# Kernel tuning notes

Hardware: AMD Instinct MI355X
Metric: run time of the kernel (lower is better)

## Reference

```python
import jax, jax.numpy as jnp
import numpy as np

B, S, DIM = 2, 2048, 2048
H, KVH, HD = 16, 8, 128
NREP = H // KVH


def _make_freqs(seqlen, head_dim):
    # Rotation-matrix form of RoPE: freqs[s,0,p] = [[cos,-sin],[sin,cos]]
    pos = jnp.arange(seqlen, dtype=jnp.float32)
    inv = 1.0 / (10000.0 ** (jnp.arange(0, head_dim, 2, dtype=jnp.float32) / head_dim))
    ang = pos[:, None] * inv[None, :]                      # (S, HD/2)
    cos, sin = jnp.cos(ang), jnp.sin(ang)
    f = jnp.stack([jnp.stack([cos, -sin], -1),
                   jnp.stack([sin, cos], -1)], -2)          # (S, HD/2, 2, 2)
    return f[:, None]                                       # (S, 1, HD/2, 2, 2)


def setup_inputs() -> dict:
    key = jax.random.key(0)
    k0, k1, k2, k3, k4 = jax.random.split(key, 5)
    x = jax.random.normal(k0, (B, S, DIM), jnp.float32)
    x_mask = jnp.ones((B, S), jnp.bool_)                    # unused by forward
    freqs_cis = _make_freqs(S, HD)
    w_qkv = jax.random.normal(k1, ((H + 2 * KVH) * HD, DIM), jnp.float32) * (DIM ** -0.5)
    w_out = jax.random.normal(k2, (DIM, H * HD), jnp.float32) * ((H * HD) ** -0.5)
    q_norm_w = 1.0 + 0.02 * jax.random.normal(k3, (HD,), jnp.float32)
    k_norm_w = 1.0 + 0.02 * jax.random.normal(k4, (HD,), jnp.float32)
    return {"x": x, "x_mask": x_mask, "freqs_cis": freqs_cis,
            "w_qkv": w_qkv, "w_out": w_out,
            "q_norm_w": q_norm_w, "k_norm_w": k_norm_w}


def _rmsnorm(x, w):
    eps = jnp.asarray(jnp.finfo(x.dtype).eps, x.dtype)
    return x * jax.lax.rsqrt(jnp.mean(x * x, -1, keepdims=True) + eps) * w


def _rope(x, freqs):
    # x: (B,S,h,HD), freqs: (S,1,HD/2,2,2)
    t = x.reshape(*x.shape[:-1], HD // 2, 1, 2)
    out = freqs[..., 0] * t[..., 0] + freqs[..., 1] * t[..., 1]
    return out.reshape(x.shape)


def reference(x, x_mask, freqs_cis, w_qkv, w_out, q_norm_w, k_norm_w):
    b, s, _ = x.shape
    qkv = jnp.einsum('bsd,od->bso', x, w_qkv)
    xq, xk, xv = jnp.split(qkv, [H * HD, (H + KVH) * HD], axis=-1)
    xq = _rope(_rmsnorm(xq.reshape(b, s, H, HD), q_norm_w), freqs_cis)
    xk = _rope(_rmsnorm(xk.reshape(b, s, KVH, HD), k_norm_w), freqs_cis)
    xv = xv.reshape(b, s, KVH, HD)
    # GQA: repeat kv heads (consecutive copies, matching unsqueeze+repeat+flatten)
    xk = jnp.repeat(xk, NREP, axis=2)
    xv = jnp.repeat(xv, NREP, axis=2)
    scale = HD ** -0.5
    scores = jnp.einsum('bqhd,bkhd->bhqk', xq, xk) * scale
    attn = jax.nn.softmax(scores, axis=-1)
    out = jnp.einsum('bhqk,bkhd->bqhd', attn, xv).reshape(b, s, H * HD)
    return jnp.einsum('bso,do->bsd', out, w_out)
```

## Files before the change

kernel.cpp:

```cpp
#include <hip/hip_runtime.h>
#include <hip/hip_bf16.h>
#include <cstdint>

typedef __bf16 bf16_t;
typedef __attribute__((ext_vector_type(8)))  __bf16 bf16x8;
typedef __attribute__((ext_vector_type(4)))  float  f32x4;
typedef __attribute__((ext_vector_type(16))) float  f32x16;

#define AS1 __attribute__((address_space(1)))
#define AS3 __attribute__((address_space(3)))
#define DEV __device__ __forceinline__

#define S_BARRIER() asm volatile("s_barrier" ::: "memory")
#define VMCNT0()    asm volatile("s_waitcnt vmcnt(0)" ::: "memory")
#define VMCNT4()    asm volatile("s_waitcnt vmcnt(4)" ::: "memory")
#define VMCNT8()    asm volatile("s_waitcnt vmcnt(8)" ::: "memory")
#define SCHED0()    __builtin_amdgcn_sched_barrier(0)

#if __has_builtin(__builtin_amdgcn_exp2f)
#define EXP2(x) __builtin_amdgcn_exp2f(x)
#else
#define EXP2(x) exp2f(x)
#endif

DEV uint32_t pk2bf(float lo, float hi) {
  union { __bf16 h[2]; uint32_t u; } x;
  x.h[0] = (__bf16)lo; x.h[1] = (__bf16)hi; return x.u;
}

__global__ __launch_bounds__(256) void k_cvt3(const float* __restrict__ s0,
                                              const float* __restrict__ s1,
                                              const float* __restrict__ s2,
                                              bf16_t* __restrict__ dst) {
  long i = (long)(blockIdx.x * 256 + threadIdx.x) * 4;
  const float* src;
  long off;
  if (i < 8388608)        { src = s0; off = i; }
  else if (i < 16777216)  { src = s1; off = i - 8388608; }
  else                    { src = s2; off = i - 16777216; }
  const float4 v = *reinterpret_cast<const float4*>(src + off);
  union { bf16_t h[4]; uint2 u; } o;
  o.h[0] = (bf16_t)v.x; o.h[1] = (bf16_t)v.y;
  o.h[2] = (bf16_t)v.z; o.h[3] = (bf16_t)v.w;
  *reinterpret_cast<uint2*>(dst + i) = o.u;
}

#define RD_A4(dst, base, MF)                                              \
  _Pragma("unroll") for (int j_ = 0; j_ < 4; ++j_)                        \
  _Pragma("unroll") for (int kk_ = 0; kk_ < 2; ++kk_) {                   \
    int p_ = (wm*128 + ((MF)+j_)*16 + c16)*128 + kk_*64 + g*16;           \
    p_ ^= ((p_>>9)&1)<<5;                                                 \
    dst[j_][kk_] = *reinterpret_cast<const bf16x8*>((const char*)(base) + p_); }

#define RD_B_ALL(dst, base)                                               \
  _Pragma("unroll") for (int i_ = 0; i_ < 4; ++i_)                        \
  _Pragma("unroll") for (int kk_ = 0; kk_ < 2; ++kk_) {                   \
    int p_ = (wn*64 + i_*16 + c16)*128 + kk_*64 + g*16;                   \
    p_ ^= ((p_>>9)&1)<<5;                                                 \
    dst[i_][kk_] = *reinterpret_cast<const bf16x8*>((const char*)(base) + p_); }

#define RD_B2(dst, base)                                                  \
  _Pragma("unroll") for (int i_ = 0; i_ < 2; ++i_)                        \
  _Pragma("unroll") for (int kk_ = 0; kk_ < 2; ++kk_) {                   \
    int p_ = (wn*32 + i_*16 + c16)*128 + kk_*64 + g*16;                   \
    p_ ^= ((p_>>9)&1)<<5;                                                 \
    dst[i_][kk_] = *reinterpret_cast<const bf16x8*>((const char*)(base) + p_); }

#define MM_Q(aa, MB, NB)                                                  \
  _Pragma("unroll") for (int j_ = 0; j_ < 4; ++j_)                        \
  _Pragma("unroll") for (int i_ = 0; i_ < 2; ++i_)                        \
  _Pragma("unroll") for (int kk_ = 0; kk_ < 2; ++kk_)                     \
    acc[(MB)+j_][(NB)+i_] = __builtin_amdgcn_mfma_f32_16x16x32_bf16(      \
        aa[j_][kk_], bF[(NB)+i_][kk_], acc[(MB)+j_][(NB)+i_], 0, 0, 0);

#define MM_OG(aa, MB)                                                     \
  _Pragma("unroll") for (int j_ = 0; j_ < 4; ++j_)                        \
  _Pragma("unroll") for (int i_ = 0; i_ < 2; ++i_)                        \
  _Pragma("unroll") for (int kk_ = 0; kk_ < 2; ++kk_)                     \
    acc[(MB)+j_][i_] = __builtin_amdgcn_mfma_f32_16x16x32_bf16(           \
        aa[j_][kk_], bG[i_][kk_], acc[(MB)+j_][i_], 0, 0, 0);

#define STAGE_A(dstbase, half, tt)                                        \
  _Pragma("unroll") for (int j_ = 0; j_ < 2; ++j_)                        \
    __builtin_amdgcn_global_load_lds(                                     \
        (const AS1 void*)(Ag + srcA[half][j_] + (tt)*64),                 \
        (AS3 void*)((char*)(dstbase) + ((half)*1024 + 512*j_ + wuni)*16), \
        16, 0, 0);

#define STAGE_B(dstbase, half, tt)                                        \
  _Pragma("unroll") for (int j_ = 0; j_ < 2; ++j_)                        \
    __builtin_amdgcn_global_load_lds(                                     \
        (const AS1 void*)(Bg + srcB[half][j_] + (tt)*64),                 \
        (AS3 void*)((char*)(dstbase) + ((half)*1024 + 512*j_ + wuni)*16), \
        16, 0, 0);

#define STAGE_B2(dstbase, tt)                                             \
  _Pragma("unroll") for (int j_ = 0; j_ < 2; ++j_)                        \
    __builtin_amdgcn_global_load_lds(                                     \
        (const AS1 void*)(Bg + srcB2[j_] + (tt)*64),                      \
        (AS3 void*)((char*)(dstbase) + (512*j_ + wuni)*16), 16, 0, 0);

__global__ __launch_bounds__(512, 2) void k_gemm256(
    const bf16_t* __restrict__ Ag, const bf16_t* __restrict__ Bg,
    void* __restrict__ Cv, int M, int N, int K, int out_bf16)
{
  extern __shared__ char smemraw[];
  const int tid = threadIdx.x;
  const int w = tid >> 6, l = tid & 63;
  const int wm = w >> 2, wn = w & 3;
  const int c16 = l & 15, g = l >> 4;
  const int wuni = tid & 0x1C0;

  const int nwg = gridDim.x, cpx = nwg >> 3;
  const int bid = blockIdx.x;
  const int L = (bid & 7) * cpx + (bid >> 3);
  const int nbx = N >> 8;
  const int m0 = (L / nbx) * 256, n0 = (L % nbx) * 256;

  int srcA[2][2], srcB[2][2];
#pragma unroll
  for (int half = 0; half < 2; ++half)
#pragma unroll
    for (int j = 0; j < 2; ++j) {
      int ch = half * 1024 + 512 * j + tid;
      int cc = ch ^ (((ch >> 5) & 1) << 1);
      int row = cc >> 3, c8 = (cc & 7) * 8;
      srcA[half][j] = (m0 + row) * K + c8;
      srcB[half][j] = (n0 + row) * K + c8;
    }

  f32x4 acc[8][4] = {};
  bf16x8 aF[4][2], bF[4][2];

  char* const Ab0 = smemraw;
  char* const Ab1 = smemraw + 32768;
  char* const Bb0 = smemraw + 65536;
  char* const Bb1 = smemraw + 98304;

  const int NT = K >> 6;

  STAGE_B(Bb0, 0, 0); STAGE_B(Bb0, 1, 0);
  STAGE_A(Ab0, 0, 0); STAGE_A(Ab0, 1, 0);
  VMCNT0();
  S_BARRIER();
  RD_B_ALL(bF, Bb0);

#pragma unroll 1
  for (int t = 0; t < NT; ++t) {
    char* const Asp = (t & 1) ? Ab1 : Ab0;
    char* const Asn = (t & 1) ? Ab0 : Ab1;
    char* const Bsn = (t & 1) ? Bb0 : Bb1;
    const bool more = (t + 1 < NT);

    VMCNT0();
    if (more) { STAGE_B(Bsn, 0, t + 1); }
    S_BARRIER();
    RD_A4(aF, Asp, 0);
    __builtin_amdgcn_s_setprio(1);
    MM_Q(aF, 0, 0);
    __builtin_amdgcn_s_setprio(0); SCHED0();
    S_BARRIER();

    if (more) { STAGE_B(Bsn, 1, t + 1); }
    S_BARRIER();
    __builtin_amdgcn_s_setprio(1);
    MM_Q(aF, 0, 2);
    __builtin_amdgcn_s_setprio(0); SCHED0();
    S_BARRIER();

    if (more) { STAGE_A(Asn, 0, t + 1); }
    S_BARRIER();
    RD_A4(aF, Asp, 4);
    __builtin_amdgcn_s_setprio(1);
    MM_Q(aF, 4, 0);
    __builtin_amdgcn_s_setprio(0); SCHED0();
    S_BARRIER();

    if (more) { STAGE_A(Asn, 1, t + 1); VMCNT4(); }
    S_BARRIER();
    __builtin_amdgcn_s_setprio(1);
    MM_Q(aF, 4, 2);
    __builtin_amdgcn_s_setprio(0); SCHED0();
    if (more) { RD_B_ALL(bF, Bsn); }
    S_BARRIER();
  }

#pragma unroll
  for (int mf = 0; mf < 8; ++mf)
#pragma unroll
    for (int nf = 0; nf < 4; ++nf) {
      const int cc = n0 + wn * 64 + nf * 16 + c16;
#pragma unroll
      for (int r = 0; r < 4; ++r) {
        const int rr = m0 + wm * 128 + mf * 16 + g * 4 + r;
        if (out_bf16)
          ((bf16_t*)Cv)[(size_t)rr * N + cc] = (bf16_t)acc[mf][nf][r];
        else
          ((float*)Cv)[(size_t)rr * N + cc] = acc[mf][nf][r];
      }
    }
}

__global__ __launch_bounds__(512, 2) void k_og(
    const bf16_t* __restrict__ Ag, const bf16_t* __restrict__ Bg,
    float* __restrict__ Cv, int M, int N, int K)
{
  extern __shared__ char smemraw[];
  const int tid = threadIdx.x;
  const int w = tid >> 6, l = tid & 63;
  const int wm = w >> 2, wn = w & 3;
  const int c16 = l & 15, g = l >> 4;
  const int wuni = tid & 0x1C0;

  const int nwg = gridDim.x, cpx = nwg >> 3;
  const int bid = blockIdx.x;
  const int L = (bid & 7) * cpx + (bid >> 3);
  const int nbx = N >> 7;
  const int m0 = (L / nbx) * 256, n0 = (L % nbx) * 128;

  int srcA[2][2], srcB2[2];
#pragma unroll
  for (int half = 0; half < 2; ++half)
#pragma unroll
    for (int j = 0; j < 2; ++j) {
      int ch = half * 1024 + 512 * j + tid;
      int cc = ch ^ (((ch >> 5) & 1) << 1);
      int row = cc >> 3, c8 = (cc & 7) * 8;
      srcA[half][j] = (m0 + row) * K + c8;
    }
#pragma unroll
  for (int j = 0; j < 2; ++j) {
    int ch = 512 * j + tid;
    int cc = ch ^ (((ch >> 5) & 1) << 1);
    int row = cc >> 3, c8 = (cc & 7) * 8;
    srcB2[j] = (n0 + row) * K + c8;
  }

  f32x4 acc[8][2] = {};
  bf16x8 aF[4][2], bG[2][2];

  char* const Ab0 = smemraw;
  char* const Ab1 = smemraw + 32768;
  char* const Bb0 = smemraw + 65536;
  char* const Bb1 = smemraw + 81920;

  const int NT = K >> 6;

  STAGE_B2(Bb0, 0);
  STAGE_A(Ab0, 0, 0); STAGE_A(Ab0, 1, 0);
  VMCNT0();
  S_BARRIER();
  RD_B2(bG, Bb0);

#pragma unroll 1
  for (int t = 0; t < NT; ++t) {
    char* const Asp = (t & 1) ? Ab1 : Ab0;
    char* const Asn = (t & 1) ? Ab0 : Ab1;
    char* const Bsn = (t & 1) ? Bb0 : Bb1;
    const bool more = (t + 1 < NT);

    VMCNT0();
    if (more) { STAGE_B2(Bsn, t + 1); STAGE_A(Asn, 0, t + 1); }
    S_BARRIER();
    RD_A4(aF, Asp, 0);
    __builtin_amdgcn_s_setprio(1);
    MM_OG(aF, 0);
    __builtin_amdgcn_s_setprio(0); SCHED0();
    S_BARRIER();

    if (more) { STAGE_A(Asn, 1, t + 1); VMCNT4(); }
    S_BARRIER();
    RD_A4(aF, Asp, 4);
    __builtin_amdgcn_s_setprio(1);
    MM_OG(aF, 4);
    __builtin_amdgcn_s_setprio(0); SCHED0();
    if (more) { RD_B2(bG, Bsn); }
    S_BARRIER();
  }

#pragma unroll
  for (int mf = 0; mf < 8; ++mf)
#pragma unroll
    for (int nf = 0; nf < 2; ++nf) {
      const int cc = n0 + wn * 32 + nf * 16 + c16;
#pragma unroll
      for (int r = 0; r < 4; ++r) {
        const int rr = m0 + wm * 128 + mf * 16 + g * 4 + r;
        Cv[(size_t)rr * N + cc] = acc[mf][nf][r];
      }
    }
}

__global__ __launch_bounds__(256) void k_prep(
    const bf16_t* __restrict__ qkv, const float* __restrict__ freqs,
    const float* __restrict__ qw, const float* __restrict__ kw,
    bf16_t* __restrict__ Qd, bf16_t* __restrict__ Kd,
    bf16_t* __restrict__ Vt)
{
  __shared__ bf16_t vt[64][136];
  const int bid = blockIdx.x;
  if (bid < 24576) {
    const int w = threadIdx.x >> 6, l = threadIdx.x & 63;
    const int R = bid * 4 + w;
    const int j = R >> 12;
    const int token = R & 4095;
    const int s = token & 2047, b = token >> 11;
    const bool isq = (j < 16);
    const int col0 = isq ? (j << 7) : (2048 + ((j - 16) << 7));

    union { uint32_t u; __bf16 h[2]; } xin;
    xin.u = *reinterpret_cast<const uint32_t*>(qkv + (size_t)token * 4096 + col0 + 2 * l);
    float x0 = (float)xin.h[0], x1 = (float)xin.h[1];
    float ss = x0 * x0 + x1 * x1;
#pragma unroll
    for (int d = 1; d < 64; d <<= 1) ss += __shfl_xor(ss, d, 64);
    const float rn = rsqrtf(ss * (1.0f / 128.0f) + 1.1920929e-7f);
    const float2 wv = *reinterpret_cast<const float2*>((isq ? qw : kw) + 2 * l);
    const float y0 = x0 * rn * wv.x, y1 = x1 * rn * wv.y;
    const float4 f = *reinterpret_cast<const float4*>(freqs + (size_t)s * 256 + l * 4);
    float o0 = f.x * y0 + f.y * y1;
    float o1 = f.z * y0 + f.w * y1;
    if (isq) { o0 *= 0.1275187989014331f; o1 *= 0.1275187989014331f; }
    const uint32_t pk = pk2bf(o0, o1);
    if (isq)
      *reinterpret_cast<uint32_t*>(Qd + ((size_t)(b * 16 + j) * 2048 + s) * 128 + 2 * l) = pk;
    else
      *reinterpret_cast<uint32_t*>(Kd + ((size_t)(b * 8 + (j - 16)) * 2048 + s) * 128 + 2 * l) = pk;
  } else {
    const int vb = bid - 24576;
    const int tid = threadIdx.x;
    const int st = vb & 31, kh = (vb >> 5) & 7, b = vb >> 8;
    const int s0 = st * 64;
#pragma unroll
    for (int i = 0; i < 4; ++i) {
      int ch = tid + 256 * i;
      int srow = ch >> 4, d8 = ch & 15;
      bf16x8 v = *reinterpret_cast<const bf16x8*>(
          qkv + (size_t)(b * 2048 + s0 + srow) * 4096 + 3072 + kh * 128 + d8 * 8);
      *reinterpret_cast<bf16x8*>(&vt[srow][d8 * 8]) = v;
    }
    __syncthreads();
    const int d = tid >> 1, sc = tid & 1;
    bf16_t* dst = Vt + ((size_t)(b * 8 + kh) * 128 + d) * 2048 + s0 + 32 * sc;
#pragma unroll
    for (int grp = 0; grp < 4; ++grp) {
      uint32_t pk[4];
#pragma unroll
      for (int q = 0; q < 4; ++q) {
        int jj = 32 * sc + grp * 8 + q * 2;
        union { __bf16 h[2]; uint32_t u; } e;
        e.h[0] = vt[jj][d]; e.h[1] = vt[jj + 1][d];
        pk[q] = e.u;
      }
      uint4 o; o.x = pk[0]; o.y = pk[1]; o.z = pk[2]; o.w = pk[3];
      *reinterpret_cast<uint4*>(dst + grp * 8) = o;
    }
  }
}

__global__ __launch_bounds__(256, 2) void k_attn(
    const bf16_t* __restrict__ Qd, const bf16_t* __restrict__ Kd,
    const bf16_t* __restrict__ Vt, bf16_t* __restrict__ O)
{
  __shared__ bf16_t kbuf[2][64 * 128];
  __shared__ bf16_t vbuf[2][128 * 64];
  const int tid = threadIdx.x;
  const int w = tid >> 6, l = tid & 63;
  const int c = l & 31, h2 = l >> 5;
  const int bid = blockIdx.x;
  const int qt = bid & 15, h = (bid >> 4) & 15, b = bid >> 8;
  const int kvh = h >> 1;
  const bf16_t* Qg = Qd + ((size_t)(b * 16 + h) * 2048 + qt * 128 + w * 32) * 128;
  const bf16_t* Kg = Kd + ((size_t)(b * 8 + kvh) * 2048) * 128;
  const bf16_t* Vg = Vt + ((size_t)(b * 8 + kvh) * 128) * 2048;

  bf16x8 qf[8];
#pragma unroll
  for (int s = 0; s < 8; ++s)
    qf[s] = *reinterpret_cast<const bf16x8*>(Qg + (size_t)c * 128 + s * 16 + h2 * 8);

  f32x16 oacc[4] = {};
  float l0 = 0.f, l1 = 0.f, l2 = 0.f, l3 = 0.f;

  auto stage = [&](int buf, int kt) {
#pragma unroll
    for (int i = 0; i < 4; ++i) {
      int ch = tid + 256 * i;
      {
        int key = ch >> 4, d16 = ch & 15;
        int soff = key * 256 + ((d16 * 16) ^ ((key & 7) << 4));
        __builtin_amdgcn_global_load_lds(
            (const AS1 void*)((const char*)Kg + (size_t)kt * 64 * 256 + soff),
            (AS3 void*)((char*)&kbuf[buf][0] + (w * 64 + 256 * i) * 16), 16, 0, 0);
      }
      {
        int d = ch >> 3, k8 = (ch & 7) ^ (d & 7);
        __builtin_amdgcn_global_load_lds(
            (const AS1 void*)(Vg + (size_t)d * 2048 + kt * 64 + k8 * 8),
            (AS3 void*)((char*)&vbuf[buf][0] + (w * 64 + 256 * i) * 16), 16, 0, 0);
      }
    }
  };

  auto compute = [&](int buf) {
    f32x16 sacc[2] = {};
    const char* kb = (const char*)&kbuf[buf][0];
    __builtin_amdgcn_s_setprio(1);
#pragma unroll
    for (int m = 0; m < 2; ++m)
#pragma unroll
      for (int s = 0; s < 8; ++s) {
        int byte = (m * 32 + c) * 256 + ((s * 32 + h2 * 16) ^ ((c & 7) << 4));
        bf16x8 kf = *reinterpret_cast<const bf16x8*>(kb + byte);
        sacc[m] = __builtin_amdgcn_mfma_f32_32x32x16_bf16(kf, qf[s], sacc[m], 0, 0, 0);
      }
    __builtin_amdgcn_s_setprio(0);

#pragma unroll
    for (int m = 0; m < 2; ++m)
#pragma unroll
      for (int r = 0; r < 16; r += 4) {
        float p0 = EXP2(sacc[m][r + 0]);
        float p1 = EXP2(sacc[m][r + 1]);
        float p2 = EXP2(sacc[m][r + 2]);
        float p3 = EXP2(sacc[m][r + 3]);
        sacc[m][r + 0] = p0; sacc[m][r + 1] = p1;
        sacc[m][r + 2] = p2; sacc[m][r + 3] = p3;
        l0 += p0; l1 += p1; l2 += p2; l3 += p3;
      }

    const char* vb = (const char*)&vbuf[buf][0];
#pragma unroll
    for (int t = 0; t < 4; ++t) {
      const int m = t >> 1, q2i = t & 1;
      uint32_t u0 = pk2bf(sacc[m][8 * q2i + 0], sacc[m][8 * q2i + 1]);
      uint32_t u1 = pk2bf(sacc[m][8 * q2i + 2], sacc[m][8 * q2i + 3]);
      uint32_t u2 = pk2bf(sacc[m][8 * q2i + 4], sacc[m][8 * q2i + 5]);
      uint32_t u3 = pk2bf(sacc[m][8 * q2i + 6], sacc[m][8 * q2i + 7]);
      auto r02 = __builtin_amdgcn_permlane32_swap((int)u0, (int)u2, false, false);
      auto r13 = __builtin_amdgcn_permlane32_swap((int)u1, (int)u3, false, false);
      union { uint32_t u[4]; bf16x8 v; } pb;
      pb.u[0] = (uint32_t)r02[0]; pb.u[1] = (uint32_t)r13[0];
      pb.u[2] = (uint32_t)r02[1]; pb.u[3] = (uint32_t)r13[1];
      __builtin_amdgcn_s_setprio(1);
#pragma unroll
      for (int df = 0; df < 4; ++df) {
        int byte = (df * 32 + c) * 128 + ((t * 32 + h2 * 16) ^ ((c & 7) << 4));
        bf16x8 vf = *reinterpret_cast<const bf16x8*>(vb + byte);
        oacc[df] = __builtin_amdgcn_mfma_f32_32x32x16_bf16(vf, pb.v, oacc[df], 0, 0, 0);
      }
      __builtin_amdgcn_s_setprio(0);
    }
  };

  stage(0, 0);
#pragma unroll 1
  for (int kt = 0; kt < 31; ++kt) {
    stage((kt + 1) & 1, kt + 1);
    VMCNT8();
    S_BARRIER();
    compute(kt & 1);
    S_BARRIER();
  }
  VMCNT0();
  S_BARRIER();
  compute(1);

  float lrun = (l0 + l1) + (l2 + l3);
  lrun += __shfl_xor(lrun, 32, 64);
  const float inv = 1.0f / lrun;
  bf16_t* Og = O + ((size_t)(b * 2048 + qt * 128 + w * 32 + c) * 2048) + h * 128;
#pragma unroll
  for (int df = 0; df < 4; ++df)
#pragma unroll
    for (int rg = 0; rg < 4; ++rg) {
      uint32_t w0 = pk2bf(oacc[df][rg * 4 + 0] * inv, oacc[df][rg * 4 + 1] * inv);
      uint32_t w1 = pk2bf(oacc[df][rg * 4 + 2] * inv, oacc[df][rg * 4 + 3] * inv);
      uint2 ww; ww.x = w0; ww.y = w1;
      *reinterpret_cast<uint2*>(Og + df * 32 + 8 * rg + 4 * h2) = ww;
    }
}

extern "C" void kernel_launch(void* const* d_in, const int* in_sizes, int n_in,
                              void* d_out, int out_size, void* d_ws, size_t ws_size,
                              hipStream_t stream)
{
  const float* x     = (const float*)d_in[0];
  const float* freqs = (const float*)d_in[2];
  const float* wqkv  = (const float*)d_in[3];
  const float* wout  = (const float*)d_in[4];
  const float* qw    = (const float*)d_in[5];
  const float* kw    = (const float*)d_in[6];
  float* out = (float*)d_out;

  bf16_t* Xb   = (bf16_t*)d_ws;
  bf16_t* Wqb  = Xb  + 8388608;
  bf16_t* Wob  = Wqb + 8388608;
  bf16_t* qkvb = Wob + 4194304;
  bf16_t* Qdp  = qkvb + 16777216;
  bf16_t* Kdp  = Qdp + 8388608;
  bf16_t* Vtp  = Kdp + 4194304;
  bf16_t* Ob   = qkvb;

  (void)hipFuncSetAttribute((const void*)k_gemm256,
                            hipFuncAttributeMaxDynamicSharedMemorySize, 131072);
  (void)hipFuncSetAttribute((const void*)k_og,
                            hipFuncAttributeMaxDynamicSharedMemorySize, 98304);

  k_cvt3<<<20480, 256, 0, stream>>>(x, wqkv, wout, Xb);
  k_gemm256<<<256, 512, 131072, stream>>>(Xb, Wqb, qkvb, 4096, 4096, 2048, 1);
  k_prep<<<25088, 256, 0, stream>>>(qkvb, freqs, qw, kw, Qdp, Kdp, Vtp);
  k_attn<<<512, 256, 0, stream>>>(Qdp, Kdp, Vtp, Ob);
  k_og<<<256, 512, 98304, stream>>>(Ob, Wob, out, 4096, 2048, 2048);
}
```

Baseline: 232.8 us.

## Process two 32-row query tiles per warp in attention, halving warps per block

The attention kernel now runs 2 warps per block instead of 4, and each warp handles 64 query rows as two 32-row MFMA tiles. Each K/V fragment read from LDS therefore feeds two MFMAs, halving LDS read traffic per unit of compute. Each thread issues twice as many async global-to-LDS loads, so the vmcnt wait is raised to match. The cost is doubled register use (two sets of Q fragments, score and output accumulators) and fewer waves per CU to hide latency, with launch bounds changed to (128,1).

Result: slower. 249.8 us (+7.3%).

```diff
diff --git a/kernel.cpp b/kernel.cpp
--- a/kernel.cpp
+++ b/kernel.cpp
@@ -14,7 +14,7 @@
 #define S_BARRIER() asm volatile("s_barrier" ::: "memory")
 #define VMCNT0()    asm volatile("s_waitcnt vmcnt(0)" ::: "memory")
 #define VMCNT4()    asm volatile("s_waitcnt vmcnt(4)" ::: "memory")
-#define VMCNT8()    asm volatile("s_waitcnt vmcnt(8)" ::: "memory")
+#define VMCNT16()   asm volatile("s_waitcnt vmcnt(16)" ::: "memory")
 #define SCHED0()    __builtin_amdgcn_sched_barrier(0)
 
 #if __has_builtin(__builtin_amdgcn_exp2f)
@@ -358,7 +358,7 @@
   }
 }
 
-__global__ __launch_bounds__(256, 2) void k_attn(
+__global__ __launch_bounds__(128, 1) void k_attn(
     const bf16_t* __restrict__ Qd, const bf16_t* __restrict__ Kd,
     const bf16_t* __restrict__ Vt, bf16_t* __restrict__ O)
 {
@@ -370,40 +370,43 @@
   const int bid = blockIdx.x;
   const int qt = bid & 15, h = (bid >> 4) & 15, b = bid >> 8;
   const int kvh = h >> 1;
-  const bf16_t* Qg = Qd + ((size_t)(b * 16 + h) * 2048 + qt * 128 + w * 32) * 128;
+  const bf16_t* Qg = Qd + ((size_t)(b * 16 + h) * 2048 + qt * 128 + w * 64) * 128;
   const bf16_t* Kg = Kd + ((size_t)(b * 8 + kvh) * 2048) * 128;
   const bf16_t* Vg = Vt + ((size_t)(b * 8 + kvh) * 128) * 2048;
 
-  bf16x8 qf[8];
-#pragma unroll
-  for (int s = 0; s < 8; ++s)
-    qf[s] = *reinterpret_cast<const bf16x8*>(Qg + (size_t)c * 128 + s * 16 + h2 * 8);
-
-  f32x16 oacc[4] = {};
-  float l0 = 0.f, l1 = 0.f, l2 = 0.f, l3 = 0.f;
+  bf16x8 qf0[8], qf1[8];
+#pragma unroll
+  for (int s = 0; s < 8; ++s) {
+    qf0[s] = *reinterpret_cast<const bf16x8*>(Qg + (size_t)c * 128 + s * 16 + h2 * 8);
+    qf1[s] = *reinterpret_cast<const bf16x8*>(Qg + (size_t)(32 + c) * 128 + s * 16 + h2 * 8);
+  }
+
+  f32x16 oacc0[4] = {}, oacc1[4] = {};
+  float la0 = 0.f, la1 = 0.f, la2 = 0.f, la3 = 0.f;
+  float lb0 = 0.f, lb1 = 0.f, lb2 = 0.f, lb3 = 0.f;
 
   auto stage = [&](int buf, int kt) {
 #pragma unroll
-    for (int i = 0; i < 4; ++i) {
-      int ch = tid + 256 * i;
+    for (int i = 0; i < 8; ++i) {
+      int ch = tid + 128 * i;
       {
         int key = ch >> 4, d16 = ch & 15;
         int soff = key * 256 + ((d16 * 16) ^ ((key & 7) << 4));
         __builtin_amdgcn_global_load_lds(
             (const AS1 void*)((const char*)Kg + (size_t)kt * 64 * 256 + soff),
-            (AS3 void*)((char*)&kbuf[buf][0] + (w * 64 + 256 * i) * 16), 16, 0, 0);
+            (AS3 void*)((char*)&kbuf[buf][0] + ch * 16), 16, 0, 0);
       }
       {
         int d = ch >> 3, k8 = (ch & 7) ^ (d & 7);
         __builtin_amdgcn_global_load_lds(
             (const AS1 void*)(Vg + (size_t)d * 2048 + kt * 64 + k8 * 8),
-            (AS3 void*)((char*)&vbuf[buf][0] + (w * 64 + 256 * i) * 16), 16, 0, 0);
+            (AS3 void*)((char*)&vbuf[buf][0] + ch * 16), 16, 0, 0);
       }
     }
   };
 
   auto compute = [&](int buf) {
-    f32x16 sacc[2] = {};
+    f32x16 s0[2] = {}, s1[2] = {};
     const char* kb = (const char*)&kbuf[buf][0];
     __builtin_amdgcn_s_setprio(1);
 #pragma unroll
@@ -412,7 +415,8 @@
       for (int s = 0; s < 8; ++s) {
         int byte = (m * 32 + c) * 256 + ((s * 32 + h2 * 16) ^ ((c & 7) << 4));
         bf16x8 kf = *reinterpret_cast<const bf16x8*>(kb + byte);
-        sacc[m] = __builtin_amdgcn_mfma_f32_32x32x16_bf16(kf, qf[s], sacc[m], 0, 0, 0);
+        s0[m] = __builtin_amdgcn_mfma_f32_32x32x16_bf16(kf, qf0[s], s0[m], 0, 0, 0);
+        s1[m] = __builtin_amdgcn_mfma_f32_32x32x16_bf16(kf, qf1[s], s1[m], 0, 0, 0);
       }
     __builtin_amdgcn_s_setprio(0);
 
@@ -420,34 +424,49 @@
     for (int m = 0; m < 2; ++m)
 #pragma unroll
       for (int r = 0; r < 16; r += 4) {
-        float p0 = EXP2(sacc[m][r + 0]);
-        float p1 = EXP2(sacc[m][r + 1]);
-        float p2 = EXP2(sacc[m][r + 2]);
-        float p3 = EXP2(sacc[m][r + 3]);
-        sacc[m][r + 0] = p0; sacc[m][r + 1] = p1;
-        sacc[m][r + 2] = p2; sacc[m][r + 3] = p3;
-        l0 += p0; l1 += p1; l2 += p2; l3 += p3;
+        float a0 = EXP2(s0[m][r + 0]);
+        float a1 = EXP2(s0[m][r + 1]);
+        float a2 = EXP2(s0[m][r + 2]);
+        float a3 = EXP2(s0[m][r + 3]);
+        s0[m][r + 0] = a0; s0[m][r + 1] = a1; s0[m][r + 2] = a2; s0[m][r + 3] = a3;
+        la0 += a0; la1 += a1; la2 += a2; la3 += a3;
+        float b0 = EXP2(s1[m][r + 0]);
+        float b1 = EXP2(s1[m][r + 1]);
+        float b2 = EXP2(s1[m][r + 2]);
+        float b3 = EXP2(s1[m][r + 3]);
+        s1[m][r + 0] = b0; s1[m][r + 1] = b1; s1[m][r + 2] = b2; s1[m][r + 3] = b3;
+        lb0 += b0; lb1 += b1; lb2 += b2; lb3 += b3;
       }
 
     const char* vb = (const char*)&vbuf[buf][0];
 #pragma unroll
     for (int t = 0; t < 4; ++t) {
       const int m = t >> 1, q2i = t & 1;
-      uint32_t u0 = pk2bf(sacc[m][8 * q2i + 0], sacc[m][8 * q2i + 1]);
-      uint32_t u1 = pk2bf(sacc[m][8 * q2i + 2], sacc[m][8 * q2i + 3]);
-      uint32_t u2 = pk2bf(sacc[m][8 * q2i + 4], sacc[m][8 * q2i + 5]);
-      uint32_t u3 = pk2bf(sacc[m][8 * q2i + 6], sacc[m][8 * q2i + 7]);
+      uint32_t u0 = pk2bf(s0[m][8 * q2i + 0], s0[m][8 * q2i + 1]);
+      uint32_t u1 = pk2bf(s0[m][8 * q2i + 2], s0[m][8 * q2i + 3]);
+      uint32_t u2 = pk2bf(s0[m][8 * q2i + 4], s0[m][8 * q2i + 5]);
+      uint32_t u3 = pk2bf(s0[m][8 * q2i + 6], s0[m][8 * q2i + 7]);
       auto r02 = __builtin_amdgcn_permlane32_swap((int)u0, (int)u2, false, false);
       auto r13 = __builtin_amdgcn_permlane32_swap((int)u1, (int)u3, false, false);
-      union { uint32_t u[4]; bf16x8 v; } pb;
-      pb.u[0] = (uint32_t)r02[0]; pb.u[1] = (uint32_t)r13[0];
-      pb.u[2] = (uint32_t)r02[1]; pb.u[3] = (uint32_t)r13[1];
+      union { uint32_t u[4]; bf16x8 v; } pb0;
+      pb0.u[0] = (uint32_t)r02[0]; pb0.u[1] = (uint32_t)r13[0];
+      pb0.u[2] = (uint32_t)r02[1]; pb0.u[3] = (uint32_t)r13[1];
+      uint32_t w0 = pk2bf(s1[m][8 * q2i + 0], s1[m][8 * q2i + 1]);
+      uint32_t w1 = pk2bf(s1[m][8 * q2i + 2], s1[m][8 * q2i + 3]);
+      uint32_t w2 = pk2bf(s1[m][8 * q2i + 4], s1[m][8 * q2i + 5]);
+      uint32_t w3 = pk2bf(s1[m][8 * q2i + 6], s1[m][8 * q2i + 7]);
+      auto t02 = __builtin_amdgcn_permlane32_swap((int)w0, (int)w2, false, false);
+      auto t13 = __builtin_amdgcn_permlane32_swap((int)w1, (int)w3, false, false);
+      union { uint32_t u[4]; bf16x8 v; } pb1;
+      pb1.u[0] = (uint32_t)t02[0]; pb1.u[1] = (uint32_t)t13[0];
+      pb1.u[2] = (uint32_t)t02[1]; pb1.u[3] = (uint32_t)t13[1];
       __builtin_amdgcn_s_setprio(1);
 #pragma unroll
       for (int df = 0; df < 4; ++df) {
         int byte = (df * 32 + c) * 128 + ((t * 32 + h2 * 16) ^ ((c & 7) << 4));
         bf16x8 vf = *reinterpret_cast<const bf16x8*>(vb + byte);
-        oacc[df] = __builtin_amdgcn_mfma_f32_32x32x16_bf16(vf, pb.v, oacc[df], 0, 0, 0);
+        oacc0[df] = __builtin_amdgcn_mfma_f32_32x32x16_bf16(vf, pb0.v, oacc0[df], 0, 0, 0);
+        oacc1[df] = __builtin_amdgcn_mfma_f32_32x32x16_bf16(vf, pb1.v, oacc1[df], 0, 0, 0);
       }
       __builtin_amdgcn_s_setprio(0);
     }
@@ -457,7 +476,7 @@
 #pragma unroll 1
   for (int kt = 0; kt < 31; ++kt) {
     stage((kt + 1) & 1, kt + 1);
-    VMCNT8();
+    VMCNT16();
     S_BARRIER();
     compute(kt & 1);
     S_BARRIER();
@@ -466,18 +485,26 @@
   S_BARRIER();
   compute(1);
 
-  float lrun = (l0 + l1) + (l2 + l3);
-  lrun += __shfl_xor(lrun, 32, 64);
-  const float inv = 1.0f / lrun;
-  bf16_t* Og = O + ((size_t)(b * 2048 + qt * 128 + w * 32 + c) * 2048) + h * 128;
+  float lrun0 = (la0 + la1) + (la2 + la3);
+  lrun0 += __shfl_xor(lrun0, 32, 64);
+  float lrun1 = (lb0 + lb1) + (lb2 + lb3);
+  lrun1 += __shfl_xor(lrun1, 32, 64);
+  const float inv0 = 1.0f / lrun0;
+  const float inv1 = 1.0f / lrun1;
+  bf16_t* Og0 = O + ((size_t)(b * 2048 + qt * 128 + w * 64 + c) * 2048) + h * 128;
+  bf16_t* Og1 = Og0 + (size_t)32 * 2048;
 #pragma unroll
   for (int df = 0; df < 4; ++df)
 #pragma unroll
     for (int rg = 0; rg < 4; ++rg) {
-      uint32_t w0 = pk2bf(oacc[df][rg * 4 + 0] * inv, oacc[df][rg * 4 + 1] * inv);
-      uint32_t w1 = pk2bf(oacc[df][rg * 4 + 2] * inv, oacc[df][rg * 4 + 3] * inv);
-      uint2 ww; ww.x = w0; ww.y = w1;
-      *reinterpret_cast<uint2*>(Og + df * 32 + 8 * rg + 4 * h2) = ww;
+      uint32_t a0 = pk2bf(oacc0[df][rg * 4 + 0] * inv0, oacc0[df][rg * 4 + 1] * inv0);
+      uint32_t a1 = pk2bf(oacc0[df][rg * 4 + 2] * inv0, oacc0[df][rg * 4 + 3] * inv0);
+      uint2 wa; wa.x = a0; wa.y = a1;
+      *reinterpret_cast<uint2*>(Og0 + df * 32 + 8 * rg + 4 * h2) = wa;
+      uint32_t b0w = pk2bf(oacc1[df][rg * 4 + 0] * inv1, oacc1[df][rg * 4 + 1] * inv1);
+      uint32_t b1w = pk2bf(oacc1[df][rg * 4 + 2] * inv1, oacc1[df][rg * 4 + 3] * inv1);
+      uint2 wb; wb.x = b0w; wb.y = b1w;
+      *reinterpret_cast<uint2*>(Og1 + df * 32 + 8 * rg + 4 * h2) = wb;
     }
 }
 
@@ -510,6 +537,6 @@
   k_cvt3<<<20480, 256, 0, stream>>>(x, wqkv, wout, Xb);
   k_gemm256<<<256, 512, 131072, stream>>>(Xb, Wqb, qkvb, 4096, 4096, 2048, 1);
   k_prep<<<25088, 256, 0, stream>>>(qkvb, freqs, qw, kw, Qdp, Kdp, Vtp);
-  k_attn<<<512, 256, 0, stream>>>(Qdp, Kdp, Vtp, Ob);
+  k_attn<<<512, 128, 0, stream>>>(Qdp, Kdp, Vtp, Ob);
   k_og<<<256, 512, 98304, stream>>>(Ob, Wob, out, 4096, 2048, 2048);
 }
```

## Triple-buffer A tiles in QKV GEMM to prefetch two K-steps ahead

Applied to the files above, without the earlier changes.

The QKV projection GEMM moves from double-buffered A and B LDS tiles to a three-slot ring for A, with A loads issued two iterations ahead while B stays one ahead. The blanket vmcnt(0) wait at the top of each iteration is dropped in favour of partial waits, so global loads can stay in flight across more compute. This needs 160KB of dynamic LDS instead of 128KB and makes the wait-count bookkeeping more delicate. If the counts are wrong, tiles could be read before they arrive.

After: 234.1 us. No clear change (+0.6%).

```diff
diff --git a/kernel.cpp b/kernel.cpp
--- a/kernel.cpp
+++ b/kernel.cpp
@@ -132,28 +132,29 @@
   f32x4 acc[8][4] = {};
   bf16x8 aF[4][2], bF[4][2];
 
-  char* const Ab0 = smemraw;
-  char* const Ab1 = smemraw + 32768;
-  char* const Bb0 = smemraw + 65536;
-  char* const Bb1 = smemraw + 98304;
+  char* const Ab = smemraw;
+  char* const Bb = smemraw + 98304;
 
   const int NT = K >> 6;
 
-  STAGE_B(Bb0, 0, 0); STAGE_B(Bb0, 1, 0);
-  STAGE_A(Ab0, 0, 0); STAGE_A(Ab0, 1, 0);
-  VMCNT0();
+  STAGE_B(Bb, 0, 0); STAGE_B(Bb, 1, 0);
+  STAGE_A(Ab, 0, 0); STAGE_A(Ab, 1, 0);
+  STAGE_A(Ab + 32768, 0, 1); STAGE_A(Ab + 32768, 1, 1);
+  VMCNT4();
   S_BARRIER();
-  RD_B_ALL(bF, Bb0);
-
+  RD_B_ALL(bF, Bb);
+
+  int aCur = 0;
 #pragma unroll 1
   for (int t = 0; t < NT; ++t) {
-    char* const Asp = (t & 1) ? Ab1 : Ab0;
-    char* const Asn = (t & 1) ? Ab0 : Ab1;
-    char* const Bsn = (t & 1) ? Bb0 : Bb1;
-    const bool more = (t + 1 < NT);
-
-    VMCNT0();
-    if (more) { STAGE_B(Bsn, 0, t + 1); }
+    char* const Asp  = Ab + aCur * 32768;
+    const int aN2    = (aCur >= 1) ? (aCur - 1) : 2;
+    char* const Asn2 = Ab + aN2 * 32768;
+    char* const Bsp  = Bb + (((t + 1) & 1) * 32768);
+    const bool m1 = (t + 1 < NT);
+    const bool m2 = (t + 2 < NT);
+
+    if (m1) { STAGE_B(Bsp, 0, t + 1); }
     S_BARRIER();
     RD_A4(aF, Asp, 0);
     __builtin_amdgcn_s_setprio(1);
@@ -161,14 +162,14 @@
     __builtin_amdgcn_s_setprio(0); SCHED0();
     S_BARRIER();
 
-    if (more) { STAGE_B(Bsn, 1, t + 1); }
+    if (m1) { STAGE_B(Bsp, 1, t + 1); }
     S_BARRIER();
     __builtin_amdgcn_s_setprio(1);
     MM_Q(aF, 0, 2);
     __builtin_amdgcn_s_setprio(0); SCHED0();
     S_BARRIER();
 
-    if (more) { STAGE_A(Asn, 0, t + 1); }
+    if (m2) { STAGE_A(Asn2, 0, t + 2); }
     S_BARRIER();
     RD_A4(aF, Asp, 4);
     __builtin_amdgcn_s_setprio(1);
@@ -176,13 +177,16 @@
     __builtin_amdgcn_s_setprio(0); SCHED0();
     S_BARRIER();
 
-    if (more) { STAGE_A(Asn, 1, t + 1); VMCNT4(); }
+    if (m2)      { STAGE_A(Asn2, 1, t + 2); VMCNT4(); }
+    else if (m1) { VMCNT0(); }
     S_BARRIER();
     __builtin_amdgcn_s_setprio(1);
     MM_Q(aF, 4, 2);
     __builtin_amdgcn_s_setprio(0); SCHED0();
-    if (more) { RD_B_ALL(bF, Bsn); }
-    S_BARRIER();
+    if (m1) { RD_B_ALL(bF, Bsp); }
+    S_BARRIER();
+
+    aCur = (aCur < 2) ? (aCur + 1) : 0;
   }
 
 #pragma unroll
@@ -503,12 +507,12 @@
   bf16_t* Ob   = qkvb;
 
   (void)hipFuncSetAttribute((const void*)k_gemm256,
-                            hipFuncAttributeMaxDynamicSharedMemorySize, 131072);
+                            hipFuncAttributeMaxDynamicSharedMemorySize, 163840);
   (void)hipFuncSetAttribute((const void*)k_og,
                             hipFuncAttributeMaxDynamicSharedMemorySize, 98304);
 
   k_cvt3<<<20480, 256, 0, stream>>>(x, wqkv, wout, Xb);
-  k_gemm256<<<256, 512, 131072, stream>>>(Xb, Wqb, qkvb, 4096, 4096, 2048, 1);
+  k_gemm256<<<256, 512, 163840, stream>>>(Xb, Wqb, qkvb, 4096, 4096, 2048, 1);
   k_prep<<<25088, 256, 0, stream>>>(qkvb, freqs, qw, kw, Qdp, Kdp, Vtp);
   k_attn<<<512, 256, 0, stream>>>(Qdp, Kdp, Vtp, Ob);
   k_og<<<256, 512, 98304, stream>>>(Ob, Wob, out, 4096, 2048, 2048);
```
